# Optimization experiments

Measured on AMD Instinct MI355X. Metric: run time of the kernel, lower is better.

The kernel has to match this reference:

```python
import jax, jax.numpy as jnp
import numpy as np

B, T, E = 64, 512, 768
H = 512            # hid_dim
NF = 256           # n_filters
FS = (3, 4, 5)     # filter_sizes


def gru_step(x, h, Wih, Whh, bih, bhh):
    # torch.nn.GRUCell math; gate order: reset, update, new
    gi = x @ Wih.T + bih
    gh = h @ Whh.T + bhh
    ir, iz, in_ = jnp.split(gi, 3, axis=-1)
    hr, hz, hn = jnp.split(gh, 3, axis=-1)
    r = jax.nn.sigmoid(ir + hr)
    z = jax.nn.sigmoid(iz + hz)
    n = jnp.tanh(in_ + r * hn)
    return (1.0 - z) * n + z * h


def setup_inputs() -> dict:
    key = jax.random.key(0)
    ks = jax.random.split(key, 32)
    s = 0.02
    inp = {
        "embedded": jax.random.normal(ks[0], (B, T, E), jnp.float32),
        "mask": jnp.ones((B, T), jnp.int32),
        # select-policy GRUCell
        "Wih_c": jax.random.normal(ks[1], (3 * H, E)) * s,
        "Whh_c": jax.random.normal(ks[2], (3 * H, H)) * s,
        "bih_c": jnp.zeros((3 * H,)),
        "bhh_c": jnp.zeros((3 * H,)),
        "Ws": jax.random.normal(ks[3], (2, H)) * s,
        "bs": jnp.zeros((2,)),
        # 2-layer GRU
        "Wih0": jax.random.normal(ks[4], (3 * H, E)) * s,
        "Whh0": jax.random.normal(ks[5], (3 * H, H)) * s,
        "bih0": jnp.zeros((3 * H,)),
        "bhh0": jnp.zeros((3 * H,)),
        "Wih1": jax.random.normal(ks[6], (3 * H, H)) * s,
        "Whh1": jax.random.normal(ks[7], (3 * H, H)) * s,
        "bih1": jnp.zeros((3 * H,)),
        "bhh1": jnp.zeros((3 * H,)),
        # convs (OIHW)
        "Wc3": jax.random.normal(ks[8], (NF, 1, 3, H)) * s,
        "bc3": jnp.zeros((NF,)),
        "Wc4": jax.random.normal(ks[9], (NF, 1, 4, H)) * s,
        "bc4": jnp.zeros((NF,)),
        "Wc5": jax.random.normal(ks[10], (NF, 1, 5, H)) * s,
        "bc5": jnp.zeros((NF,)),
        # output linear
        "Wo": jax.random.normal(ks[11], (1, len(FS) * NF)) * s,
        "bo": jnp.zeros((1,)),
    }
    return inp


def reference(embedded, mask, Wih_c, Whh_c, bih_c, bhh_c, Ws, bs,
              Wih0, Whh0, bih0, bhh0, Wih1, Whh1, bih1, bhh1,
              Wc3, bc3, Wc4, bc4, Wc5, bc5, Wo, bo):
    b, t, _ = embedded.shape
    emb = jax.lax.stop_gradient(embedded)  # policy uses detached embeddings
    lens = mask.sum(axis=1).astype(jnp.int32)  # [B]

    # --- select_policy (eval mode: argmax selection), batched scan over time ---
    def sel_step(h, x_t):
        h = gru_step(x_t, h, Wih_c, Whh_c, bih_c, bhh_c)
        logits = h @ Ws.T + bs  # [B, 2]
        return h, jnp.argmax(logits, axis=-1).astype(jnp.int32)

    h0 = jnp.zeros((b, Whh_c.shape[1]), emb.dtype)
    _, ks = jax.lax.scan(sel_step, h0, jnp.swapaxes(emb, 0, 1))  # [T, B]
    sel = ks.T  # [B, T]
    t_idx = jnp.arange(t)[None, :]
    sel = jnp.where(t_idx == 0, 1, sel)                  # first token always kept
    sel = jnp.where(t_idx == lens[:, None] - 1, 1, sel)  # last valid token kept
    sel = jnp.where(t_idx >= lens[:, None], 0, sel)      # padding never kept
    nsel = sel.sum(axis=1)  # [B] lengths of compacted sequences

    # compact selected tokens to the front (stable argsort trick)
    order = jnp.argsort(1 - sel, axis=1, stable=True)  # [B, T]
    new_emb = jnp.take_along_axis(emb, order[:, :, None], axis=1)
    valid = t_idx < nsel[:, None]  # [B, T]
    new_emb = new_emb * valid[:, :, None].astype(emb.dtype)

    # --- 2-layer GRU over packed (= masked, left-aligned) sequences ---
    def run_layer(x, Wih, Whh, bih, bhh):
        def step(h, inputs):
            x_t, m_t = inputs
            hn = gru_step(x_t, h, Wih, Whh, bih, bhh)
            h = jnp.where(m_t[:, None], hn, h)
            return h, jnp.where(m_t[:, None], hn, jnp.zeros_like(hn))
        hh = jnp.zeros((x.shape[0], Whh.shape[1]), x.dtype)
        _, ys = jax.lax.scan(step, hh, (jnp.swapaxes(x, 0, 1), valid.T))
        return jnp.swapaxes(ys, 0, 1)  # [B, T, H]

    out = run_layer(new_emb, Wih0, Whh0, bih0, bhh0)
    out = run_layer(out, Wih1, Whh1, bih1, bhh1)

    # --- Kim-CNN head ---
    xc = out[:, None, :, :]  # [B, 1, T, H]
    pooled = []
    for Wc, bc in ((Wc3, bc3), (Wc4, bc4), (Wc5, bc5)):
        c = jax.lax.conv_general_dilated(
            xc, Wc, (1, 1), 'VALID',
            dimension_numbers=('NCHW', 'OIHW', 'NCHW'))  # [B, NF, T-fs+1, 1]
        c = jax.nn.relu(c + bc[None, :, None, None])[..., 0]
        pooled.append(jnp.max(c, axis=2))  # [B, NF]
    cat = jnp.concatenate(pooled, axis=1)  # dropout is identity in eval
    return (cat @ Wo.T + bo)[:, 0]  # [B]
```

## Files before the change

kernel.cpp:

```cpp
#include <hip/hip_runtime.h>
#include <hip/hip_bf16.h>
#include <cstddef>

constexpr int B_ = 64, T_ = 512, E_ = 768, H_ = 512, G_ = 1536, NF_ = 256;

typedef float f32x4 __attribute__((ext_vector_type(4)));
typedef __bf16 bf16x8 __attribute__((ext_vector_type(8)));

constexpr size_t SZ_GIC   = (size_t)B_ * T_ * G_ * 4;
constexpr size_t OFF_GI   = 0;
constexpr size_t OFF_OUT  = (size_t)B_ * T_ * G_ * 2;
constexpr size_t OFF_WBF0 = 170u * 1024 * 1024;
constexpr size_t OFF_WBF1 = OFF_WBF0 + (size_t)G_ * H_ * 2;
constexpr size_t OFF_WIH0 = OFF_WBF1 + (size_t)G_ * H_ * 2;
constexpr size_t OFF_WIH1 = OFF_WIH0 + (size_t)G_ * E_ * 2;
constexpr size_t OFF_WC3  = OFF_WIH1 + (size_t)G_ * H_ * 2;
constexpr size_t OFF_WC4  = OFF_WC3 + (size_t)NF_ * 3 * H_ * 2;
constexpr size_t OFF_WC5  = OFF_WC4 + (size_t)NF_ * 4 * H_ * 2;
constexpr size_t OFF_MISC = SZ_GIC;
constexpr size_t OFF_H0   = OFF_MISC;
constexpr size_t OFF_H1   = OFF_H0 + (size_t)B_ * H_ * 4;
constexpr size_t OFF_SEL  = OFF_H1 + (size_t)B_ * H_ * 4;
constexpr size_t OFF_ORD  = OFF_SEL + (size_t)B_ * T_ * 4;
constexpr size_t OFF_NSEL = OFF_ORD + (size_t)B_ * T_ * 4;
constexpr size_t OFF_MAXN = OFF_NSEL + 256;
constexpr size_t OFF_FLG  = OFF_MAXN + 256;
constexpr size_t OFF_JOBS = OFF_FLG + 512;
constexpr size_t OFF_POOL = OFF_FLG + 1024;
constexpr size_t OFF_RING0 = OFF_POOL + (size_t)B_ * 3 * NF_ * 4;
constexpr size_t OFF_RING1 = OFF_RING0 + 4ull * 64 * 512 * 2;
constexpr size_t WS_NEED  = OFF_RING1 + 4ull * 64 * 1536 * 2;

constexpr int WP_N0 = G_ * H_;
constexpr int WP_N1 = WP_N0 + G_ * H_;
constexpr int WP_N2 = WP_N1 + G_ * E_;
constexpr int WP_N3 = WP_N2 + G_ * H_;
constexpr int WP_N4 = WP_N3 + NF_ * 3 * H_;
constexpr int WP_N5 = WP_N4 + NF_ * 4 * H_;
constexpr int WP_N6 = WP_N5 + NF_ * 5 * H_;

#define CLOAD4(dst, ptr) \
    asm volatile("global_load_dwordx4 %0, %1, off sc0 sc1" : "=v"(dst) : "v"(ptr))
#define CLOAD2(dst, ptr) \
    asm volatile("global_load_dwordx2 %0, %1, off sc0 sc1" : "=v"(dst) : "v"(ptr))
#define CWAIT() do { \
    asm volatile("s_waitcnt vmcnt(0)" ::: "memory"); \
    __builtin_amdgcn_sched_barrier(0); } while (0)
#define CSTORE4(ptr, val) \
    asm volatile("global_store_dword %0, %1, off sc0 sc1" :: "v"(ptr), "v"(val) : "memory")
#define CSTORE8(ptr, val) \
    asm volatile("global_store_dwordx2 %0, %1, off sc0 sc1" :: "v"(ptr), "v"(val) : "memory")
#define CSTORE2(ptr, val) \
// ... 22 lines not shown
            __builtin_amdgcn_s_sleep(1);
        }
    }
    __syncthreads();
}

template<int N>
__device__ __forceinline__ void poll_ge(const int* flags, int thresh, int tid) {
    if (tid < 64) {
        const int idx = (tid < N) ? tid : 0;
        int v;
        for (;;) {
            asm volatile("global_load_dword %0, %1, off sc0 sc1\n\t"
                         "s_waitcnt vmcnt(0)"
                         : "=v"(v) : "v"(flags + idx) : "memory");
            if (__all(v >= thresh)) break;
            __builtin_amdgcn_s_sleep(1);
        }
    }
    __syncthreads();
}

__device__ __forceinline__ void poll_cnt(const int* p, int thr) {
    int v;
    for (;;) {
        asm volatile("global_load_dword %0, %1, off sc0 sc1\n\t"
                     "s_waitcnt vmcnt(0)"
                     : "=v"(v) : "v"(p) : "memory");
        if (__all(v >= thr)) break;
        __builtin_amdgcn_s_sleep(1);
    }
}

__device__ __forceinline__ void bar_wait128(const int* flags, int t, int tid) {
    if (tid < 64) {
        int v1, v2;
        for (;;) {
            asm volatile("global_load_dword %0, %2, off sc0 sc1\n\t"
                         "global_load_dword %1, %3, off sc0 sc1\n\t"
                         "s_waitcnt vmcnt(0)"
                         : "=&v"(v1), "=&v"(v2)
                         : "v"(flags + tid), "v"(flags + tid + 64) : "memory");
            if (__all((v1 >= t) && (v2 >= t))) break;
            __builtin_amdgcn_s_sleep(1);
        }
    }
    __syncthreads();
}

__device__ __forceinline__ void bar_arrive(int* flags, int t, int tid, int idx) {
    asm volatile("s_waitcnt vmcnt(0)" ::: "memory");
    __syncthreads();
    if (tid == 0) { int pv = t + 1; CSTORE4(flags + idx, pv); }
}

template<int AMODE, int OMODE>
__global__ __launch_bounds__(256) void gemm_mfma(
    const float* __restrict__ A, const unsigned short* __restrict__ Wb,
    const float* __restrict__ bias,
    unsigned short* __restrict__ Cb, unsigned int* __restrict__ pool,
    int N, int K, int ldA, int rowsPerB, int tilesPerB, int nb,
    const int* __restrict__ order, const int* __restrict__ nsel, int poolOff)
{
    __shared__ __align__(16) unsigned short As[64][40];
    __shared__ __align__(16) unsigned short Bs[64][40];
    __shared__ const float* rowp[64];

    const int tid = threadIdx.x;
    const int l = tid & 63;
    const int q = tid >> 6;
    const int per = 16 * nb;
    const int id = blockIdx.x;
    const int sup = id / per, rr2 = id % per;
    const int mblk = sup * 16 + (rr2 & 15);
    const int n0 = (rr2 >> 4) * 64;

    int tileb = 0, tilet0 = 0;
    if (AMODE != 0) { tileb = mblk / tilesPerB; tilet0 = (mblk % tilesPerB) * 64; }

    if (tid < 64) {
        const float* p = nullptr;
        if (AMODE == 0) {
            p = A + ((size_t)mblk * 64 + tid) * (size_t)ldA;
        } else if (AMODE == 1) {
            int t = tilet0 + tid;
            if (t < nsel[tileb]) {
                int src = order[tileb * T_ + t];
                p = A + ((size_t)tileb * T_ + src) * (size_t)ldA;
            }
        } else {
            int t = tilet0 + tid;
            if (t < rowsPerB) p = A + ((size_t)tileb * T_ + t) * (size_t)ldA;
        }
        rowp[tid] = p;
    }
    __syncthreads();

    f32x4 acc0 = {0.f,0.f,0.f,0.f}, acc1 = {0.f,0.f,0.f,0.f};
    f32x4 acc2 = {0.f,0.f,0.f,0.f}, acc3 = {0.f,0.f,0.f,0.f};

    const int r = tid & 63, seg = tid >> 6;
    const float* ap = rowp[r];
    if (ap) ap += seg * 8;
    const unsigned short* wrow = Wb + (size_t)(n0 + r) * (size_t)K + seg * 8;

    for (int k0 = 0; k0 < K; k0 += 32) {
        float4 fa = make_float4(0,0,0,0), fb = make_float4(0,0,0,0);
        if (ap) { fa = *(const float4*)(ap + k0); fb = *(const float4*)(ap + k0 + 4); }
        const uint4 wv = *(const uint4*)(wrow + k0);
        __syncthreads();
        uint4 pk;
        pk.x = (unsigned)f2bu(fa.x) | ((unsigned)f2bu(fa.y) << 16);
        pk.y = (unsigned)f2bu(fa.z) | ((unsigned)f2bu(fa.w) << 16);
        pk.z = (unsigned)f2bu(fb.x) | ((unsigned)f2bu(fb.y) << 16);
        pk.w = (unsigned)f2bu(fb.z) | ((unsigned)f2bu(fb.w) << 16);
        *(uint4*)&As[r][seg * 8] = pk;
        *(uint4*)&Bs[r][seg * 8] = wv;
        __syncthreads();
        const bf16x8 av = *(const bf16x8*)&As[q * 16 + (l & 15)][(l >> 4) * 8];
        const bf16x8 b0 = *(const bf16x8*)&Bs[ 0 + (l & 15)][(l >> 4) * 8];
        const bf16x8 b1 = *(const bf16x8*)&Bs[16 + (l & 15)][(l >> 4) * 8];
        const bf16x8 b2 = *(const bf16x8*)&Bs[32 + (l & 15)][(l >> 4) * 8];
// ... 8 lines not shown
    if (OMODE == 0) {
        const int mbase = (AMODE == 0) ? mblk * 64 : tileb * T_ + tilet0;
        #pragma unroll
        for (int s = 0; s < 4; ++s) {
            const int col = n0 + s * 16 + (l & 15);
            const float bv = bias[col];
            #pragma unroll
            for (int reg = 0; reg < 4; ++reg) {
                const int m = mbase + q * 16 + (l >> 4) * 4 + reg;
                Cb[(size_t)m * (size_t)N + col] = f2bu(accs[s][reg] + bv);
            }
        }
    } else {
        #pragma unroll
        for (int s = 0; s < 4; ++s) {
            const int col = n0 + s * 16 + (l & 15);
            const float bv = bias[col];
            float mx = 0.f;
            #pragma unroll
            for (int reg = 0; reg < 4; ++reg) {
                const int t = tilet0 + q * 16 + (l >> 4) * 4 + reg;
                const float val = fmaxf(accs[s][reg] + bv, 0.f);
                if (t < rowsPerB) mx = fmaxf(mx, val);
            }
            mx = fmaxf(mx, __shfl_xor(mx, 16));
            mx = fmaxf(mx, __shfl_xor(mx, 32));
            if (l < 16)
                atomicMax(&pool[(size_t)tileb * (3*NF_) + poolOff + n0 + s*16 + l],
                          __float_as_uint(mx));
        }
    }
}

__global__ void wprep_all(
    const float* __restrict__ w0, const float* __restrict__ w1,
    const float* __restrict__ w2, const float* __restrict__ w3,
    const float* __restrict__ w4, const float* __restrict__ w5,
    const float* __restrict__ w6, unsigned short* __restrict__ o)
{
    const int i = blockIdx.x * 256 + threadIdx.x;
    if (i >= WP_N6) return;
    float v;
    if      (i < WP_N0) v = w0[i];
    else if (i < WP_N1) v = w1[i - WP_N0];
    else if (i < WP_N2) v = w2[i - WP_N1];
    else if (i < WP_N3) v = w3[i - WP_N2];
    else if (i < WP_N4) v = w4[i - WP_N3];
    else if (i < WP_N5) v = w5[i - WP_N4];
    else                v = w6[i - WP_N5];
    o[i] = f2bu(v);
}

__device__ __forceinline__ void gates_abs(
    const float* __restrict__ hs, int b, int base,
    const float* __restrict__ wR, const float* __restrict__ wZ,
    const float* __restrict__ wN,
    float& aR, float& aZ, float& aN)
{
    #pragma unroll 4
    for (int kq = 0; kq < 32; ++kq) {
        const int k = base + kq * 4;
        const float hv0 = hs[(k+0)*64 + b];
        const float hv1 = hs[(k+1)*64 + b];
        const float hv2 = hs[(k+2)*64 + b];
        const float hv3 = hs[(k+3)*64 + b];
        const float4 wr = *(const float4*)(wR + k);
        const float4 wz = *(const float4*)(wZ + k);
        const float4 wn = *(const float4*)(wN + k);
        aR = fmaf(hv0, wr.x, aR); aR = fmaf(hv1, wr.y, aR);
        aR = fmaf(hv2, wr.z, aR); aR = fmaf(hv3, wr.w, aR);
        aZ = fmaf(hv0, wz.x, aZ); aZ = fmaf(hv1, wz.y, aZ);
        aZ = fmaf(hv2, wz.z, aZ); aZ = fmaf(hv3, wz.w, aZ);
        aN = fmaf(hv0, wn.x, aN); aN = fmaf(hv1, wn.y, aN);
        aN = fmaf(hv2, wn.z, aN); aN = fmaf(hv3, wn.w, aN);
    }
}

__device__ __forceinline__ void dot_abs(
    const float* __restrict__ hs, int b, int base,
    const float* __restrict__ dWl, float& dot)
{
    #pragma unroll 4
    for (int kq = 0; kq < 16; ++kq) {
        const int k = base + kq * 4;
        const float hv0 = hs[(k+0)*64 + b];
        const float hv1 = hs[(k+1)*64 + b];
        const float hv2 = hs[(k+2)*64 + b];
        const float hv3 = hs[(k+3)*64 + b];
        const float4 dv = *(const float4*)(dWl + k);
        dot = fmaf(hv0, dv.x, dot); dot = fmaf(hv1, dv.y, dot);
        dot = fmaf(hv2, dv.z, dot); dot = fmaf(hv3, dv.w, dot);
    }
}

__global__ __launch_bounds__(512) void sel_fused(
    const float* __restrict__ emb, const float* __restrict__ Wih_c,
    const float* __restrict__ bih_c, float* __restrict__ giC,
    const float* __restrict__ Whh, const float* __restrict__ bhh,
    const float* __restrict__ Ws, const float* __restrict__ bs,
    float* __restrict__ h0, float* __restrict__ h1,
    unsigned long long* __restrict__ selm, int* __restrict__ flags,
    int* __restrict__ jobs)
{
    __shared__ __align__(16) char smem[162816];
    const int tid = threadIdx.x;
    const int bx = blockIdx.x;

    if (bx >= 128) {
        const int p = bx - 128;
        float* As = (float*)smem;
        float* Bs = As + 16 * 68;
        const int half = tid >> 8;
        const int t2 = tid & 255;
        const int srl = t2 >> 2, skl = (t2 & 3) * 4;
        const int ty = tid >> 4;
        const int tx = tid & 15;

        for (int c = 0; c < 8; ++c) {
            for (int j = p; j < 1536; j += 128) {
                const int b = j / 24, n = j % 24;
                const int mblk = b * 8 + c;
                const int n0 = n * 64;
                const float* src = (half == 0)
                    ? emb + ((size_t)mblk * 64 + srl) * (size_t)E_ + skl
                    : Wih_c + ((size_t)(n0 + srl)) * (size_t)E_ + skl;
                float* dl = (half == 0) ? As : Bs;

                float acc[2][4] = {};
                for (int k0 = 0; k0 < E_; k0 += 16) {
                    const float4 v = *(const float4*)(src + k0);
                    __syncthreads();
                    dl[(skl+0)*68 + srl] = v.x; dl[(skl+1)*68 + srl] = v.y;
                    dl[(skl+2)*68 + srl] = v.z; dl[(skl+3)*68 + srl] = v.w;
                    __syncthreads();
                    #pragma unroll
                    for (int kk = 0; kk < 16; ++kk) {
                        const float a0 = As[kk*68 + ty*2 + 0];
                        const float a1 = As[kk*68 + ty*2 + 1];
                        const float4 w4 = *(const float4*)&Bs[kk*68 + tx*4];
                        acc[0][0]=fmaf(a0,w4.x,acc[0][0]); acc[0][1]=fmaf(a0,w4.y,acc[0][1]);
                        acc[0][2]=fmaf(a0,w4.z,acc[0][2]); acc[0][3]=fmaf(a0,w4.w,acc[0][3]);
                        acc[1][0]=fmaf(a1,w4.x,acc[1][0]); acc[1][1]=fmaf(a1,w4.y,acc[1][1]);
                        acc[1][2]=fmaf(a1,w4.z,acc[1][2]); acc[1][3]=fmaf(a1,w4.w,acc[1][3]);
                    }
                }
                const float4 bv = *(const float4*)(bih_c + n0 + tx*4);
                f32x4 o0, o1;
                o0[0] = acc[0][0]+bv.x; o0[1] = acc[0][1]+bv.y;
                o0[2] = acc[0][2]+bv.z; o0[3] = acc[0][3]+bv.w;
                o1[0] = acc[1][0]+bv.x; o1[1] = acc[1][1]+bv.y;
                o1[2] = acc[1][2]+bv.z; o1[3] = acc[1][3]+bv.w;
                const float* d0 = giC + (size_t)(mblk * 64 + ty*2) * (size_t)G_ + n0 + tx*4;
                CSTOREX4(d0, o0);
                CSTOREX4(d0 + G_, o1);
                asm volatile("s_waitcnt vmcnt(0)" ::: "memory");
                __syncthreads();
                if (tid == 0)
                    __hip_atomic_fetch_add(jobs + c, 1, __ATOMIC_RELAXED,
                                           __HIP_MEMORY_SCOPE_AGENT);
                __syncthreads();
            }
        }
        return;
    }

    float* Wl    = (float*)smem;
    float* dWl   = Wl + 6144;
    float* hs    = dWl + 512;
    float* partR = hs + 32768;
    float* partZ = partR + 256;
    float* partN = partZ + 256;
    float* pdot  = partN + 256;

    const int b = tid & 63;
    const int w = __builtin_amdgcn_readfirstlane(tid >> 6);
    const int u = w >> 1, s = w & 1;
    const int iu = bx * 4 + u;

    for (int idx = tid; idx < 12 * 512; idx += 512) {
        int rr = idx >> 9, k = idx & 511;
        int ul = rr / 3, gate = rr - ul * 3;
        Wl[idx] = Whh[((size_t)gate * 512 + bx * 4 + ul) * 512 + k];
    }
    dWl[tid] = Ws[512 + tid] - Ws[tid];
    __syncthreads();

    const float bR = bhh[iu], bZ = bhh[512 + iu], bN = bhh[1024 + iu];
    const float db = bs[1] - bs[0];
    const float* __restrict__ wR = Wl + (u*3 + 0) * 512;
    const float* __restrict__ wZ = Wl + (u*3 + 1) * 512;
    const float* __restrict__ wN = Wl + (u*3 + 2) * 512;

    float pgR = 0.f, pgZ = 0.f, pgN = 0.f;
    int ready_chunk = 0;
    if (s == 0) {
        poll_cnt(jobs + 0, 1536);
        ready_chunk = 1;
        const float* gp = giC + (size_t)b * T_ * G_;
        asm volatile("global_load_dword %0, %3, off sc0 sc1\n\t"
                     "global_load_dword %1, %4, off sc0 sc1\n\t"
                     "global_load_dword %2, %5, off sc0 sc1\n\t"
                     "s_waitcnt vmcnt(0)"
                     : "=&v"(pgR), "=&v"(pgZ), "=&v"(pgN)
                     : "v"(gp + iu), "v"(gp + 512 + iu), "v"(gp + 1024 + iu)
                     : "memory");
    }

    for (int t = 0; t <= T_; ++t) {
        const bool comp = (t < T_);
        const float* hcur = (t & 1) ? h1 : h0;
        float* hnxt = (t & 1) ? h0 : h1;

        if (t > 0) bar_wait128(flags, t, tid);

        const float* hc = hcur + (size_t)tid * 4;
        float* hd = hs + tid * 4;
        float4 a0,a1,a2,a3,a4,a5,a6,a7,a8,a9,aa,ab,ac,ad,ae,af;
        CLOAD4(a0, hc +  0*2048); CLOAD4(a1, hc +  1*2048);
        CLOAD4(a2, hc +  2*2048); CLOAD4(a3, hc +  3*2048);
        CLOAD4(a4, hc +  4*2048); CLOAD4(a5, hc +  5*2048);
        CLOAD4(a6, hc +  6*2048); CLOAD4(a7, hc +  7*2048);
        CLOAD4(a8, hc +  8*2048); CLOAD4(a9, hc +  9*2048);
        CLOAD4(aa, hc + 10*2048); CLOAD4(ab, hc + 11*2048);
        CLOAD4(ac, hc + 12*2048); CLOAD4(ad, hc + 13*2048);
        CLOAD4(ae, hc + 14*2048); CLOAD4(af, hc + 15*2048);
        CWAIT();
        *(float4*)(hd +  0*2048) = a0; *(float4*)(hd +  1*2048) = a1;
        *(float4*)(hd +  2*2048) = a2; *(float4*)(hd +  3*2048) = a3;
        *(float4*)(hd +  4*2048) = a4; *(float4*)(hd +  5*2048) = a5;
        *(float4*)(hd +  6*2048) = a6; *(float4*)(hd +  7*2048) = a7;
        *(float4*)(hd +  8*2048) = a8; *(float4*)(hd +  9*2048) = a9;
// ... 5 lines not shown
        float aR = (s == 0) ? bR : 0.f;
        float aZ = (s == 0) ? bZ : 0.f;
        float aN = (s == 0) ? bN : 0.f;
        float dot = 0.f, hp = 0.f;

        if (comp) {
            gates_abs(hs, b, s * 128,       wR, wZ, wN, aR, aZ, aN);
            gates_abs(hs, b, 256 + s * 128, wR, wZ, wN, aR, aZ, aN);
            if (s == 0) hp = hs[iu * 64 + b];
        }
        dot_abs(hs, b, (w < 4) ? w * 64 : 256 + (w - 4) * 64, dWl, dot);

        if (comp && s == 1) {
            partR[u*64 + b] = aR; partZ[u*64 + b] = aZ; partN[u*64 + b] = aN;
        }
        pdot[w*64 + b] = dot;
        __syncthreads();

        if (comp && s == 0) {
            aR += partR[u*64 + b]; aZ += partZ[u*64 + b]; aN += partN[u*64 + b];
            const float r = sigm(pgR + aR);
            const float z = sigm(pgZ + aZ);
            const float n = tanhf(pgN + r * aN);
            const float hn = (1.f - z) * n + z * hp;
            const float* hdst = hnxt + (size_t)iu * 64 + b;
            CSTORE4(hdst, hn);
        }

        if (t < T_) {
            bar_arrive(flags, t, tid, bx);
            if (s == 0 && t + 1 < T_) {
                const int nc = (t + 1) >> 6;
                if (nc >= ready_chunk) { poll_cnt(jobs + nc, 1536); ready_chunk = nc + 1; }
                const float* gp = giC + ((size_t)b * T_ + t + 1) * G_;
                asm volatile("global_load_dword %0, %3, off sc0 sc1\n\t"
                             "global_load_dword %1, %4, off sc0 sc1\n\t"
                             "global_load_dword %2, %5, off sc0 sc1\n\t"
                             "s_waitcnt vmcnt(0)"
                             : "=&v"(pgR), "=&v"(pgZ), "=&v"(pgN)
                             : "v"(gp + iu), "v"(gp + 512 + iu), "v"(gp + 1024 + iu)
                             : "memory");
            }
        }
        if (w == 0 && t >= 1) {
            float p2 = pdot[0*64 + b];
            p2 += pdot[1*64 + b]; p2 += pdot[2*64 + b]; p2 += pdot[3*64 + b];
            p2 += pdot[4*64 + b]; p2 += pdot[5*64 + b]; p2 += pdot[6*64 + b];
            p2 += pdot[7*64 + b];
            unsigned long long m = __ballot((p2 + db) > 0.f);
            if (tid == 0 && bx == 0) selm[t - 1] = m;
        }
    }
}

template<int ROLE>
__device__ __forceinline__ void layer_body(
    int wg, int tid,
    const unsigned short* __restrict__ gi0,
    const unsigned short* __restrict__ ring1,
    unsigned short* __restrict__ ring0,
    const unsigned short* __restrict__ wbf, const float* __restrict__ bhh,
    const int* __restrict__ nselp, const int* __restrict__ maxnp,
    unsigned short* __restrict__ hA, unsigned short* __restrict__ hB,
    float* __restrict__ outp,
    int* __restrict__ flagsSelf, const int* __restrict__ flagsB,
    unsigned char* ldsW, unsigned char* ldsH, float* gbuf)
{
    const int l = tid & 63;
    const int q = tid >> 6;
    const int i0 = wg * 16;
    const int b = tid & 63;

    for (int idx = tid; idx < 48 * 64; idx += 256) {
        const int r = idx >> 6, seg = idx & 63;
        const int tier = r >> 4, ul = r & 15;
        const float4 v = *(const float4*)((const char*)wbf
            + ((size_t)(tier * 512 + i0 + ul) * 512) * 2 + seg * 16);
        *(float4*)(ldsW + r * 1040 + seg * 16) = v;
    }
    const float4 bRv = *(const float4*)(bhh + i0 + 4 * q);
    const float4 bZv = *(const float4*)(bhh + 512 + i0 + 4 * q);
    const float4 bNv = *(const float4*)(bhh + 1024 + i0 + 4 * q);
    const int ns = nselp[b];
    const int TOTAL = *maxnp;

    const unsigned short* gbase = gi0 + (size_t)b * T_ * (size_t)G_ + i0 + 4 * q;
    uint2 gR, gZ, gN;
    if (ROLE == 0) {
        gR = *(const uint2*)(gbase);
        gZ = *(const uint2*)(gbase + 512);
        gN = *(const uint2*)(gbase + 1024);
    }
    __syncthreads();

    for (int t = 0; t < TOTAL; ++t) {
        const unsigned short* hcur = (t & 1) ? hB : hA;
        unsigned short* hnxt = (t & 1) ? hA : hB;

        if (t > 0) bar_wait<32>(flagsSelf, t, tid);
        if (ROLE == 0) {
            if (t >= 4) poll_ge<24>(flagsB, t - 3, tid);
        } else {
            poll_ge<24>(flagsB, t + 1, tid);
            const unsigned short* gp = ring1 + ((size_t)(t & 3) * 64 + b) * G_ + i0 + 4 * q;
            CLOAD2(gR, gp); CLOAD2(gZ, gp + 512); CLOAD2(gN, gp + 1024);
        }

        {
            const char* src = (const char*)hcur + tid * 256;
            float4 s0, s1, s2, s3, s4, s5, s6, s7, s8, s9, sa, sb_, sc, sd, se, sf;
            CLOAD4(s0, src + 0 * 16);  CLOAD4(s1, src + 1 * 16);
            CLOAD4(s2, src + 2 * 16);  CLOAD4(s3, src + 3 * 16);
            CLOAD4(s4, src + 4 * 16);  CLOAD4(s5, src + 5 * 16);
            CLOAD4(s6, src + 6 * 16);  CLOAD4(s7, src + 7 * 16);
            CLOAD4(s8, src + 8 * 16);  CLOAD4(s9, src + 9 * 16);
            CLOAD4(sa, src + 10 * 16); CLOAD4(sb_, src + 11 * 16);
            CLOAD4(sc, src + 12 * 16); CLOAD4(sd, src + 13 * 16);
            CLOAD4(se, src + 14 * 16); CLOAD4(sf, src + 15 * 16);
            CWAIT();
            char* dst = (char*)ldsH + (tid >> 2) * 1040 + (tid & 3) * 256;
            *(float4*)(dst + 0 * 16) = s0;  *(float4*)(dst + 1 * 16) = s1;
            *(float4*)(dst + 2 * 16) = s2;  *(float4*)(dst + 3 * 16) = s3;
            *(float4*)(dst + 4 * 16) = s4;  *(float4*)(dst + 5 * 16) = s5;
            *(float4*)(dst + 6 * 16) = s6;  *(float4*)(dst + 7 * 16) = s7;
// ... 46 lines not shown
            float4 o;
            unsigned short ob[4];
            #pragma unroll
            for (int j = 0; j < 4; ++j) {
                const int u2 = 4 * q + j;
                const float hr = gbuf[u2 * 66 + b]        + bRv[j];
                const float hz = gbuf[(16 + u2) * 66 + b] + bZv[j];
                const float hn = gbuf[(32 + u2) * 66 + b] + bNv[j];
                const float rr = sigm(irv[j] + hr);
                const float zz = sigm(izv[j] + hz);
                const float nn = tanhf(inv[j] + rr * hn);
                const float hpf = b2f(hpb[j]);
                float hv = (1.f - zz) * nn + zz * hpf;
                if (t >= ns) hv = hpf;
                ((float*)&o)[j] = hv;
                ob[j] = f2bu(hv);
            }
            uint2 hpk;
            hpk.x = (unsigned)ob[0] | ((unsigned)ob[1] << 16);
            hpk.y = (unsigned)ob[2] | ((unsigned)ob[3] << 16);
            if (ROLE == 0) {
                const unsigned short* rdst = ring0 + ((size_t)(t & 3) * 64 + b) * 512 + i0 + 4 * q;
                CSTORE8(rdst, hpk);
            } else {
                if (t < ns)
                    *(float4*)(outp + ((size_t)b * T_ + t) * 512 + i0 + 4 * q) = o;
            }
            const unsigned short* hdst = hnxt + (size_t)b * 512 + i0 + 4 * q;
            CSTORE8(hdst, hpk);
        }

        bar_arrive(flagsSelf, t, tid, wg);
        if (ROLE == 0 && t + 1 < TOTAL) {
            const unsigned short* gp = gbase + (size_t)(t + 1) * G_;
            gR = *(const uint2*)gp;
            gZ = *(const uint2*)(gp + 512);
            gN = *(const uint2*)(gp + 1024);
        }
    }
}

__global__ __launch_bounds__(256) void rec_fused(
    const unsigned short* __restrict__ gi0,
    const unsigned short* __restrict__ wbf0,
    const unsigned short* __restrict__ wbf1,
    const unsigned short* __restrict__ wih1b,
    const float* __restrict__ bhh0, const float* __restrict__ bhh1,
    const float* __restrict__ bih1,
    const int* __restrict__ nselp, const int* __restrict__ maxnp,
    unsigned short* __restrict__ h0A, unsigned short* __restrict__ h1A,
    unsigned short* __restrict__ h0C, unsigned short* __restrict__ h1C,
    unsigned short* __restrict__ ring0, unsigned short* __restrict__ ring1,
    float* __restrict__ outp,
    int* __restrict__ flagsA, int* __restrict__ flagsB, int* __restrict__ flagsC)
{
    __shared__ __align__(16) unsigned char ldsX[64 * 1040];
    __shared__ __align__(16) unsigned char ldsY[64 * 1040];
    __shared__ float gbuf[48 * 66];

    const int tid = threadIdx.x;
    const int bx = blockIdx.x;

    if (bx < 32) {
        layer_body<0>(bx, tid, gi0, nullptr, ring0, wbf0, bhh0, nselp, maxnp,
                      h0A, h1A, nullptr, flagsA, flagsB, ldsX, ldsY, gbuf);
    } else if (bx < 56) {
        const int wg = bx - 32;
        const int l = tid & 63;
        const int q = tid >> 6;
        const int n0 = wg * 64;

        for (int idx = tid; idx < 64 * 64; idx += 256) {
            const int r = idx >> 6, seg = idx & 63;
            const float4 v = *(const float4*)((const char*)wih1b
                + ((size_t)(n0 + r) * 512) * 2 + seg * 16);
            *(float4*)(ldsX + r * 1040 + seg * 16) = v;
        }
        float bv[4];
        #pragma unroll
        for (int s = 0; s < 4; ++s) bv[s] = bih1[n0 + s * 16 + (l & 15)];
        const int TOTAL = *maxnp;
        __syncthreads();

        for (int t = 0; t < TOTAL; ++t) {
            poll_ge<32>(flagsA, t + 1, tid);
            if (t >= 4) poll_ge<32>(flagsC, t - 3, tid);

            {
                const char* src = (const char*)ring0 + (size_t)(t & 3) * 65536 + tid * 256;
                float4 s0, s1, s2, s3, s4, s5, s6, s7, s8, s9, sa, sb_, sc, sd, se, sf;
                CLOAD4(s0, src + 0 * 16);  CLOAD4(s1, src + 1 * 16);
                CLOAD4(s2, src + 2 * 16);  CLOAD4(s3, src + 3 * 16);
                CLOAD4(s4, src + 4 * 16);  CLOAD4(s5, src + 5 * 16);
                CLOAD4(s6, src + 6 * 16);  CLOAD4(s7, src + 7 * 16);
                CLOAD4(s8, src + 8 * 16);  CLOAD4(s9, src + 9 * 16);
                CLOAD4(sa, src + 10 * 16); CLOAD4(sb_, src + 11 * 16);
                CLOAD4(sc, src + 12 * 16); CLOAD4(sd, src + 13 * 16);
// ... 14 lines not shown
            f32x4 acc0 = {0.f,0.f,0.f,0.f}, acc1 = {0.f,0.f,0.f,0.f};
            f32x4 acc2 = {0.f,0.f,0.f,0.f}, acc3 = {0.f,0.f,0.f,0.f};
            {
                const char* ab2 = (const char*)ldsY + (q * 16 + (l & 15)) * 1040 + (l >> 4) * 16;
                const char* bb = (const char*)ldsX + (l & 15) * 1040 + (l >> 4) * 16;
                #pragma unroll
                for (int ks = 0; ks < 16; ++ks) {
                    const bf16x8 av = *(const bf16x8*)(ab2 + ks * 64);
                    const bf16x8 b0 = *(const bf16x8*)(bb + ks * 64);
                    const bf16x8 b1 = *(const bf16x8*)(bb + 16 * 1040 + ks * 64);
                    const bf16x8 b2 = *(const bf16x8*)(bb + 32 * 1040 + ks * 64);
                    const bf16x8 b3 = *(const bf16x8*)(bb + 48 * 1040 + ks * 64);
                    acc0 = __builtin_amdgcn_mfma_f32_16x16x32_bf16(av, b0, acc0, 0, 0, 0);
                    acc1 = __builtin_amdgcn_mfma_f32_16x16x32_bf16(av, b1, acc1, 0, 0, 0);
                    acc2 = __builtin_amdgcn_mfma_f32_16x16x32_bf16(av, b2, acc2, 0, 0, 0);
                    acc3 = __builtin_amdgcn_mfma_f32_16x16x32_bf16(av, b3, acc3, 0, 0, 0);
                }
            }
            f32x4 accs[4] = {acc0, acc1, acc2, acc3};
            #pragma unroll
            for (int s = 0; s < 4; ++s) {
                const int col = n0 + s * 16 + (l & 15);
                #pragma unroll
                for (int reg = 0; reg < 4; ++reg) {
                    const int m = q * 16 + (l >> 4) * 4 + reg;
                    const unsigned val = f2bu(accs[s][reg] + bv[s]);
                    const unsigned short* dst = ring1 + ((size_t)(t & 3) * 64 + m) * G_ + col;
                    CSTORE2(dst, val);
                }
            }
            bar_arrive(flagsB, t, tid, wg);
        }
    } else {
        layer_body<1>(bx - 56, tid, nullptr, ring1, nullptr, wbf1, bhh1, nselp, maxnp,
                      h0C, h1C, outp, flagsC, flagsB, ldsX, ldsY, gbuf);
    }
}

__global__ void build_order_k(const int* __restrict__ mask,
                              const unsigned long long* __restrict__ selm,
                              int* __restrict__ order, int* __restrict__ nsel,
                              int* __restrict__ maxn)
{
    const int b = threadIdx.x;
    int lens = 0;
    for (int t = 0; t < T_; ++t) lens += (mask[b * T_ + t] != 0);
    int cnt = 0;
    for (int t = 0; t < T_; ++t) {
        int s = (int)((selm[t] >> b) & 1ull);
        if (t == 0) s = 1;
        if (t == lens - 1) s = 1;
        if (t >= lens) s = 0;
        if (s) order[b * T_ + (cnt++)] = t;
    }
    nsel[b] = cnt;
    int c2 = cnt;
    for (int t = 0; t < T_; ++t) {
        int s = (int)((selm[t] >> b) & 1ull);
        if (t == 0) s = 1;
        if (t == lens - 1) s = 1;
        if (t >= lens) s = 0;
        if (!s) order[b * T_ + (c2++)] = t;
    }
    __shared__ int red[64];
    red[b] = cnt;
    __syncthreads();
    if (b == 0) {
// ... 16 lines not shown

extern "C" void kernel_launch(void* const* d_in, const int* in_sizes, int n_in,
                              void* d_out, int out_size, void* d_ws, size_t ws_size,
                              hipStream_t stream)
{
    (void)in_sizes; (void)n_in; (void)out_size;
    const float* emb   = (const float*)d_in[0];
    const int*   mask  = (const int*)d_in[1];
    const float* Wih_c = (const float*)d_in[2];
    const float* Whh_c = (const float*)d_in[3];
    const float* bih_c = (const float*)d_in[4];
    const float* bhh_c = (const float*)d_in[5];
    const float* Ws    = (const float*)d_in[6];
    const float* bs    = (const float*)d_in[7];
    const float* Wih0  = (const float*)d_in[8];
    const float* Whh0  = (const float*)d_in[9];
    const float* bih0  = (const float*)d_in[10];
    const float* bhh0  = (const float*)d_in[11];
    const float* Wih1  = (const float*)d_in[12];
    const float* Whh1  = (const float*)d_in[13];
    const float* bih1  = (const float*)d_in[14];
    const float* bhh1  = (const float*)d_in[15];
    const float* Wc3   = (const float*)d_in[16];
    const float* bc3   = (const float*)d_in[17];
    const float* Wc4   = (const float*)d_in[18];
    const float* bc4   = (const float*)d_in[19];
    const float* Wc5   = (const float*)d_in[20];
    const float* bc5   = (const float*)d_in[21];
    const float* Wo    = (const float*)d_in[22];
    const float* bo    = (const float*)d_in[23];

    if (ws_size < WS_NEED) return;
    char* ws = (char*)d_ws;
    float*          giC    = (float*)(ws + OFF_GI);
    unsigned short* giB    = (unsigned short*)(ws + OFF_GI);
    float*          outbuf = (float*)(ws + OFF_OUT);
    unsigned short* wpack  = (unsigned short*)(ws + OFF_WBF0);
    unsigned short* wbf0   = (unsigned short*)(ws + OFF_WBF0);
    unsigned short* wbf1   = (unsigned short*)(ws + OFF_WBF1);
    unsigned short* wih0b  = (unsigned short*)(ws + OFF_WIH0);
    unsigned short* wih1b  = (unsigned short*)(ws + OFF_WIH1);
    unsigned short* wc3b   = (unsigned short*)(ws + OFF_WC3);
    unsigned short* wc4b   = (unsigned short*)(ws + OFF_WC4);
    unsigned short* wc5b   = (unsigned short*)(ws + OFF_WC5);
    float*          h0f    = (float*)(ws + OFF_H0);
    float*          h1f    = (float*)(ws + OFF_H1);
    unsigned short* h0A    = (unsigned short*)(ws + OFF_H0);
    unsigned short* h1A    = (unsigned short*)(ws + OFF_H0 + 65536);
    unsigned short* h0C    = (unsigned short*)(ws + OFF_H0 + 131072);
    unsigned short* h1C    = (unsigned short*)(ws + OFF_H0 + 196608);
    unsigned long long* selm = (unsigned long long*)(ws + OFF_SEL);
    int*            order  = (int*)(ws + OFF_ORD);
    int*            nsel   = (int*)(ws + OFF_NSEL);
    int*            maxn   = (int*)(ws + OFF_MAXN);
    int*            flagsA = (int*)(ws + OFF_FLG);
    int*            flagsB = (int*)(ws + OFF_FLG + 128);
    int*            flagsC = (int*)(ws + OFF_FLG + 256);
    int*            jobs   = (int*)(ws + OFF_JOBS);
    unsigned int*   pool   = (unsigned int*)(ws + OFF_POOL);
    unsigned short* ring0  = (unsigned short*)(ws + OFF_RING0);
    unsigned short* ring1  = (unsigned short*)(ws + OFF_RING1);

    hipMemsetAsync(flagsA, 0, 1024, stream);
    hipMemsetAsync(h0f, 0, (size_t)B_ * H_ * 4, stream);
    sel_fused<<<256, 512, 0, stream>>>(emb, Wih_c, bih_c, giC, Whh_c, bhh_c,
                                       Ws, bs, h0f, h1f, selm, flagsA, jobs);
    build_order_k<<<1, 64, 0, stream>>>(mask, selm, order, nsel, maxn);
    wprep_all<<<(WP_N6 + 255) / 256, 256, 0, stream>>>(Whh0, Whh1, Wih0, Wih1,
                                                       Wc3, Wc4, Wc5, wpack);
    gemm_mfma<1,0><<<dim3(512 * 24), 256, 0, stream>>>(emb, wih0b, bih0, giB, nullptr,
                                                       G_, E_, E_, T_, 8, 24, order, nsel, 0);
    hipMemsetAsync(flagsA, 0, 512, stream);
    hipMemsetAsync(h0A, 0, 65536, stream);
    hipMemsetAsync(h0C, 0, 65536, stream);
    hipMemsetAsync(outbuf, 0, (size_t)B_ * T_ * H_ * 4, stream);
    rec_fused<<<88, 256, 0, stream>>>(giB, wbf0, wbf1, wih1b, bhh0, bhh1, bih1,
                                      nsel, maxn, h0A, h1A, h0C, h1C,
                                      ring0, ring1, outbuf, flagsA, flagsB, flagsC);
    hipMemsetAsync(pool, 0, (size_t)B_ * 3 * NF_ * 4, stream);
    gemm_mfma<2,1><<<dim3(512 * 4), 256, 0, stream>>>(outbuf, wc3b, bc3, nullptr, pool,
                                                      NF_, 3*H_, H_, 510, 8, 4, nullptr, nullptr, 0);
    gemm_mfma<2,1><<<dim3(512 * 4), 256, 0, stream>>>(outbuf, wc4b, bc4, nullptr, pool,
                                                      NF_, 4*H_, H_, 509, 8, 4, nullptr, nullptr, 256);
    gemm_mfma<2,1><<<dim3(512 * 4), 256, 0, stream>>>(outbuf, wc5b, bc5, nullptr, pool,
                                                      NF_, 5*H_, H_, 508, 8, 4, nullptr, nullptr, 512);
    final_k<<<1, 64, 0, stream>>>(pool, Wo, bo, (float*)d_out);
}
```

Before: 9.703 ms.

## Overlap layer-0 input projection and weight prep with select-policy recurrence

The producer blocks of sel_fused now compute the full layer-0 input projection (emb×Wih0, in FP32 FMA, stored as bf16) for every timestep and do the bf16 weight packing while the select-policy recurrence runs. This removes the separate wprep and gather MFMA GEMM launches. The select-policy input projection now goes into a 128-row-per-batch ring buffer, with producers waiting on recurrence progress flags before overwriting entries, which shrinks the workspace. Layer 0 then gathers its gi rows through the order index. The trade-offs are that all T rows are projected instead of only the selected ones, scalar FMA replaces MFMA for that GEMM, and the ring adds a producer-consumer dependency.

```diff
diff --git a/kernel.cpp b/kernel.cpp
--- a/kernel.cpp
+++ b/kernel.cpp
@@ -7,17 +7,17 @@
 typedef float f32x4 __attribute__((ext_vector_type(4)));
 typedef __bf16 bf16x8 __attribute__((ext_vector_type(8)));
 
-constexpr size_t SZ_GIC   = (size_t)B_ * T_ * G_ * 4;
-constexpr size_t OFF_GI   = 0;
-constexpr size_t OFF_OUT  = (size_t)B_ * T_ * G_ * 2;
-constexpr size_t OFF_WBF0 = 170u * 1024 * 1024;
+constexpr size_t OFF_RING_GI = 0;
+constexpr size_t OFF_OUT     = 0;
+constexpr size_t OFF_GIFULL  = 64ull * 1024 * 1024;
+constexpr size_t OFF_WBF0    = 160ull * 1024 * 1024;
 constexpr size_t OFF_WBF1 = OFF_WBF0 + (size_t)G_ * H_ * 2;
 constexpr size_t OFF_WIH0 = OFF_WBF1 + (size_t)G_ * H_ * 2;
 constexpr size_t OFF_WIH1 = OFF_WIH0 + (size_t)G_ * E_ * 2;
 constexpr size_t OFF_WC3  = OFF_WIH1 + (size_t)G_ * H_ * 2;
 constexpr size_t OFF_WC4  = OFF_WC3 + (size_t)NF_ * 3 * H_ * 2;
 constexpr size_t OFF_WC5  = OFF_WC4 + (size_t)NF_ * 4 * H_ * 2;
-constexpr size_t OFF_MISC = SZ_GIC;
+constexpr size_t OFF_MISC = 192ull * 1024 * 1024;
 constexpr size_t OFF_H0   = OFF_MISC;
 constexpr size_t OFF_H1   = OFF_H0 + (size_t)B_ * H_ * 4;
 constexpr size_t OFF_SEL  = OFF_H1 + (size_t)B_ * H_ * 4;
@@ -106,7 +106,7 @@
     }
 }
 
-__device__ __forceinline__ void bar_wait128(const int* flags, int t, int tid) {
+__device__ __forceinline__ void poll128_ge(const int* flags, int thr, int tid) {
     if (tid < 64) {
         int v1, v2;
         for (;;) {
@@ -115,11 +115,15 @@
                          "s_waitcnt vmcnt(0)"
                          : "=&v"(v1), "=&v"(v2)
                          : "v"(flags + tid), "v"(flags + tid + 64) : "memory");
-            if (__all((v1 >= t) && (v2 >= t))) break;
+            if (__all((v1 >= thr) && (v2 >= thr))) break;
             __builtin_amdgcn_s_sleep(1);
         }
     }
     __syncthreads();
+}
+
+__device__ __forceinline__ void bar_wait128(const int* flags, int t, int tid) {
+    poll128_ge(flags, t, tid);
 }
 
 __device__ __forceinline__ void bar_arrive(int* flags, int t, int tid, int idx) {
@@ -156,12 +160,6 @@
         const float* p = nullptr;
         if (AMODE == 0) {
             p = A + ((size_t)mblk * 64 + tid) * (size_t)ldA;
-        } else if (AMODE == 1) {
-            int t = tilet0 + tid;
-            if (t < nsel[tileb]) {
-                int src = order[tileb * T_ + t];
-                p = A + ((size_t)tileb * T_ + src) * (size_t)ldA;
-            }
         } else {
             int t = tilet0 + tid;
             if (t < rowsPerB) p = A + ((size_t)tileb * T_ + t) * (size_t)ldA;
@@ -236,23 +234,61 @@
     }
 }
 
-__global__ void wprep_all(
-    const float* __restrict__ w0, const float* __restrict__ w1,
-    const float* __restrict__ w2, const float* __restrict__ w3,
-    const float* __restrict__ w4, const float* __restrict__ w5,
-    const float* __restrict__ w6, unsigned short* __restrict__ o)
+template<bool TORING>
+__device__ __forceinline__ void prod_job(
+    int mblk, int n0, int ringRowBase,
+    const float* __restrict__ emb, const float* __restrict__ W,
+    const float* __restrict__ bias,
+    float* __restrict__ ring, unsigned short* __restrict__ full,
+    float* As, float* Bs, int tid)
 {
-    const int i = blockIdx.x * 256 + threadIdx.x;
-    if (i >= WP_N6) return;
-    float v;
-    if      (i < WP_N0) v = w0[i];
-    else if (i < WP_N1) v = w1[i - WP_N0];
-    else if (i < WP_N2) v = w2[i - WP_N1];
-    else if (i < WP_N3) v = w3[i - WP_N2];
-    else if (i < WP_N4) v = w4[i - WP_N3];
-    else if (i < WP_N5) v = w5[i - WP_N4];
-    else                v = w6[i - WP_N5];
-    o[i] = f2bu(v);
+    const int half = tid >> 8;
+    const int t2 = tid & 255;
+    const int srl = t2 >> 2, skl = (t2 & 3) * 4;
+    const int ty = tid >> 4, tx = tid & 15;
+    const float* src = (half == 0)
+        ? emb + ((size_t)mblk * 64 + srl) * (size_t)E_ + skl
+        : W + ((size_t)(n0 + srl)) * (size_t)E_ + skl;
+    float* dl = (half == 0) ? As : Bs;
+
+    float acc[2][4] = {};
+    for (int k0 = 0; k0 < E_; k0 += 16) {
+        const float4 v = *(const float4*)(src + k0);
+        __syncthreads();
+        dl[(skl+0)*68 + srl] = v.x; dl[(skl+1)*68 + srl] = v.y;
+        dl[(skl+2)*68 + srl] = v.z; dl[(skl+3)*68 + srl] = v.w;
+        __syncthreads();
+        #pragma unroll
+        for (int kk = 0; kk < 16; ++kk) {
+            const float a0 = As[kk*68 + ty*2 + 0];
+            const float a1 = As[kk*68 + ty*2 + 1];
+            const float4 w4 = *(const float4*)&Bs[kk*68 + tx*4];
+            acc[0][0]=fmaf(a0,w4.x,acc[0][0]); acc[0][1]=fmaf(a0,w4.y,acc[0][1]);
+            acc[0][2]=fmaf(a0,w4.z,acc[0][2]); acc[0][3]=fmaf(a0,w4.w,acc[0][3]);
+            acc[1][0]=fmaf(a1,w4.x,acc[1][0]); acc[1][1]=fmaf(a1,w4.y,acc[1][1]);
+            acc[1][2]=fmaf(a1,w4.z,acc[1][2]); acc[1][3]=fmaf(a1,w4.w,acc[1][3]);
+        }
+    }
+    const float4 bv = *(const float4*)(bias + n0 + tx*4);
+    if (TORING) {
+        f32x4 o0, o1;
+        o0[0] = acc[0][0]+bv.x; o0[1] = acc[0][1]+bv.y;
+        o0[2] = acc[0][2]+bv.z; o0[3] = acc[0][3]+bv.w;
+        o1[0] = acc[1][0]+bv.x; o1[1] = acc[1][1]+bv.y;
+        o1[2] = acc[1][2]+bv.z; o1[3] = acc[1][3]+bv.w;
+        const float* d0 = ring + (size_t)(ringRowBase + ty*2) * (size_t)G_ + n0 + tx*4;
+        CSTOREX4(d0, o0);
+        CSTOREX4(d0 + G_, o1);
+    } else {
+        ushort4 s0, s1;
+        s0.x = f2bu(acc[0][0]+bv.x); s0.y = f2bu(acc[0][1]+bv.y);
+        s0.z = f2bu(acc[0][2]+bv.z); s0.w = f2bu(acc[0][3]+bv.w);
+        s1.x = f2bu(acc[1][0]+bv.x); s1.y = f2bu(acc[1][1]+bv.y);
+        s1.z = f2bu(acc[1][2]+bv.z); s1.w = f2bu(acc[1][3]+bv.w);
+        unsigned short* d0 = full + (size_t)(mblk * 64 + ty*2) * (size_t)G_ + n0 + tx*4;
+        *(ushort4*)d0 = s0;
+        *(ushort4*)(d0 + G_) = s1;
+    }
 }
 
 __device__ __forceinline__ void gates_abs(
@@ -299,12 +335,18 @@
 
 __global__ __launch_bounds__(512) void sel_fused(
     const float* __restrict__ emb, const float* __restrict__ Wih_c,
-    const float* __restrict__ bih_c, float* __restrict__ giC,
+    const float* __restrict__ bih_c, float* __restrict__ ring,
     const float* __restrict__ Whh, const float* __restrict__ bhh,
     const float* __restrict__ Ws, const float* __restrict__ bs,
     float* __restrict__ h0, float* __restrict__ h1,
     unsigned long long* __restrict__ selm, int* __restrict__ flags,
-    int* __restrict__ jobs)
+    int* __restrict__ jobs,
+    const float* __restrict__ Wih0, const float* __restrict__ bih0,
+    unsigned short* __restrict__ giFull,
+    const float* __restrict__ Whh0, const float* __restrict__ Whh1,
+    const float* __restrict__ Wih1,
+    const float* __restrict__ Wc3, const float* __restrict__ Wc4,
+    const float* __restrict__ Wc5, unsigned short* __restrict__ wpack)
 {
     __shared__ __align__(16) char smem[162816];
     const int tid = threadIdx.x;
@@ -314,49 +356,12 @@
         const int p = bx - 128;
         float* As = (float*)smem;
         float* Bs = As + 16 * 68;
-        const int half = tid >> 8;
-        const int t2 = tid & 255;
-        const int srl = t2 >> 2, skl = (t2 & 3) * 4;
-        const int ty = tid >> 4;
-        const int tx = tid & 15;
-
-        for (int c = 0; c < 8; ++c) {
+
+        for (int c = 0; c < 2; ++c) {
             for (int j = p; j < 1536; j += 128) {
                 const int b = j / 24, n = j % 24;
-                const int mblk = b * 8 + c;
-                const int n0 = n * 64;
-                const float* src = (half == 0)
-                    ? emb + ((size_t)mblk * 64 + srl) * (size_t)E_ + skl
-                    : Wih_c + ((size_t)(n0 + srl)) * (size_t)E_ + skl;
-                float* dl = (half == 0) ? As : Bs;
-
-                float acc[2][4] = {};
-                for (int k0 = 0; k0 < E_; k0 += 16) {
-                    const float4 v = *(const float4*)(src + k0);
-                    __syncthreads();
-                    dl[(skl+0)*68 + srl] = v.x; dl[(skl+1)*68 + srl] = v.y;
-                    dl[(skl+2)*68 + srl] = v.z; dl[(skl+3)*68 + srl] = v.w;
-                    __syncthreads();
-                    #pragma unroll
-                    for (int kk = 0; kk < 16; ++kk) {
-                        const float a0 = As[kk*68 + ty*2 + 0];
-                        const float a1 = As[kk*68 + ty*2 + 1];
-                        const float4 w4 = *(const float4*)&Bs[kk*68 + tx*4];
-                        acc[0][0]=fmaf(a0,w4.x,acc[0][0]); acc[0][1]=fmaf(a0,w4.y,acc[0][1]);
-                        acc[0][2]=fmaf(a0,w4.z,acc[0][2]); acc[0][3]=fmaf(a0,w4.w,acc[0][3]);
-                        acc[1][0]=fmaf(a1,w4.x,acc[1][0]); acc[1][1]=fmaf(a1,w4.y,acc[1][1]);
-                        acc[1][2]=fmaf(a1,w4.z,acc[1][2]); acc[1][3]=fmaf(a1,w4.w,acc[1][3]);
-                    }
-                }
-                const float4 bv = *(const float4*)(bih_c + n0 + tx*4);
-                f32x4 o0, o1;
-                o0[0] = acc[0][0]+bv.x; o0[1] = acc[0][1]+bv.y;
-                o0[2] = acc[0][2]+bv.z; o0[3] = acc[0][3]+bv.w;
-                o1[0] = acc[1][0]+bv.x; o1[1] = acc[1][1]+bv.y;
-                o1[2] = acc[1][2]+bv.z; o1[3] = acc[1][3]+bv.w;
-                const float* d0 = giC + (size_t)(mblk * 64 + ty*2) * (size_t)G_ + n0 + tx*4;
-                CSTOREX4(d0, o0);
-                CSTOREX4(d0 + G_, o1);
+                prod_job<true>(b * 8 + c, n * 64, b * 128 + (c & 1) * 64,
+                               emb, Wih_c, bih_c, ring, nullptr, As, Bs, tid);
                 asm volatile("s_waitcnt vmcnt(0)" ::: "memory");
                 __syncthreads();
                 if (tid == 0)
@@ -364,6 +369,48 @@
                                            __HIP_MEMORY_SCOPE_AGENT);
                 __syncthreads();
             }
+        }
+        int fg = 0;
+        for (int c = 2; c < 8; ++c) {
+            if (fg < 8) {
+                for (int j = p; j < 1536; j += 128) {
+                    const int b = j / 24, n = j % 24;
+                    prod_job<false>(b * 8 + fg, n * 64, 0,
+                                    emb, Wih0, bih0, nullptr, giFull, As, Bs, tid);
+                }
+                ++fg;
+            }
+            poll128_ge(flags, 64 * (c - 1), tid);
+            for (int j = p; j < 1536; j += 128) {
+                const int b = j / 24, n = j % 24;
+                prod_job<true>(b * 8 + c, n * 64, b * 128 + (c & 1) * 64,
+                               emb, Wih_c, bih_c, ring, nullptr, As, Bs, tid);
+                asm volatile("s_waitcnt vmcnt(0)" ::: "memory");
+                __syncthreads();
+                if (tid == 0)
+                    __hip_atomic_fetch_add(jobs + c, 1, __ATOMIC_RELAXED,
+                                           __HIP_MEMORY_SCOPE_AGENT);
+                __syncthreads();
+            }
+        }
+        while (fg < 8) {
+            for (int j = p; j < 1536; j += 128) {
+                const int b = j / 24, n = j % 24;
+                prod_job<false>(b * 8 + fg, n * 64, 0,
+                                emb, Wih0, bih0, nullptr, giFull, As, Bs, tid);
+            }
+            ++fg;
+        }
+        for (int i = p * 512 + tid; i < WP_N6; i += 128 * 512) {
+            float v;
+            if      (i < WP_N0) v = Whh0[i];
+            else if (i < WP_N1) v = Whh1[i - WP_N0];
+            else if (i < WP_N2) v = Wih0[i - WP_N1];
+            else if (i < WP_N3) v = Wih1[i - WP_N2];
+            else if (i < WP_N4) v = Wc3[i - WP_N3];
+            else if (i < WP_N5) v = Wc4[i - WP_N4];
+            else                v = Wc5[i - WP_N5];
+            wpack[i] = f2bu(v);
         }
         return;
     }
@@ -400,7 +447,7 @@
     if (s == 0) {
         poll_cnt(jobs + 0, 1536);
         ready_chunk = 1;
-        const float* gp = giC + (size_t)b * T_ * G_;
+        const float* gp = ring + (size_t)(b * 128) * G_;
         asm volatile("global_load_dword %0, %3, off sc0 sc1\n\t"
                      "global_load_dword %1, %4, off sc0 sc1\n\t"
                      "global_load_dword %2, %5, off sc0 sc1\n\t"
@@ -472,7 +519,7 @@
             if (s == 0 && t + 1 < T_) {
                 const int nc = (t + 1) >> 6;
                 if (nc >= ready_chunk) { poll_cnt(jobs + nc, 1536); ready_chunk = nc + 1; }
-                const float* gp = giC + ((size_t)b * T_ + t + 1) * G_;
+                const float* gp = ring + (size_t)(b * 128 + ((t + 1) & 127)) * G_;
                 asm volatile("global_load_dword %0, %3, off sc0 sc1\n\t"
                              "global_load_dword %1, %4, off sc0 sc1\n\t"
                              "global_load_dword %2, %5, off sc0 sc1\n\t"
@@ -497,6 +544,7 @@
 __device__ __forceinline__ void layer_body(
     int wg, int tid,
     const unsigned short* __restrict__ gi0,
+    const int* __restrict__ order,
     const unsigned short* __restrict__ ring1,
     unsigned short* __restrict__ ring0,
     const unsigned short* __restrict__ wbf, const float* __restrict__ bhh,
@@ -524,12 +572,13 @@
     const int ns = nselp[b];
     const int TOTAL = *maxnp;
 
-    const unsigned short* gbase = gi0 + (size_t)b * T_ * (size_t)G_ + i0 + 4 * q;
     uint2 gR, gZ, gN;
     if (ROLE == 0) {
-        gR = *(const uint2*)(gbase);
-        gZ = *(const uint2*)(gbase + 512);
-        gN = *(const uint2*)(gbase + 1024);
+        const int oi = order[b * T_];
+        const unsigned short* gp = gi0 + ((size_t)b * T_ + oi) * (size_t)G_ + i0 + 4 * q;
+        gR = *(const uint2*)gp;
+        gZ = *(const uint2*)(gp + 512);
+        gN = *(const uint2*)(gp + 1024);
     }
     __syncthreads();
 
@@ -642,7 +691,8 @@
 
         bar_arrive(flagsSelf, t, tid, wg);
         if (ROLE == 0 && t + 1 < TOTAL) {
-            const unsigned short* gp = gbase + (size_t)(t + 1) * G_;
+            const int oi = order[b * T_ + (t + 1)];
+            const unsigned short* gp = gi0 + ((size_t)b * T_ + oi) * (size_t)G_ + i0 + 4 * q;
             gR = *(const uint2*)gp;
             gZ = *(const uint2*)(gp + 512);
             gN = *(const uint2*)(gp + 1024);
@@ -651,7 +701,7 @@
 }
 
 __global__ __launch_bounds__(256) void rec_fused(
-    const unsigned short* __restrict__ gi0,
+    const unsigned short* __restrict__ giFull, const int* __restrict__ order,
     const unsigned short* __restrict__ wbf0,
     const unsigned short* __restrict__ wbf1,
     const unsigned short* __restrict__ wih1b,
@@ -672,7 +722,7 @@
     const int bx = blockIdx.x;
 
     if (bx < 32) {
-        layer_body<0>(bx, tid, gi0, nullptr, ring0, wbf0, bhh0, nselp, maxnp,
+        layer_body<0>(bx, tid, giFull, order, nullptr, ring0, wbf0, bhh0, nselp, maxnp,
                       h0A, h1A, nullptr, flagsA, flagsB, ldsX, ldsY, gbuf);
     } else if (bx < 56) {
         const int wg = bx - 32;
@@ -753,7 +803,7 @@
             bar_arrive(flagsB, t, tid, wg);
         }
     } else {
-        layer_body<1>(bx - 56, tid, nullptr, ring1, nullptr, wbf1, bhh1, nselp, maxnp,
+        layer_body<1>(bx - 56, tid, nullptr, nullptr, ring1, nullptr, wbf1, bhh1, nselp, maxnp,
                       h0C, h1C, outp, flagsC, flagsB, ldsX, ldsY, gbuf);
     }
 }
@@ -836,13 +886,12 @@
 
     if (ws_size < WS_NEED) return;
     char* ws = (char*)d_ws;
-    float*          giC    = (float*)(ws + OFF_GI);
-    unsigned short* giB    = (unsigned short*)(ws + OFF_GI);
+    float*          ring   = (float*)(ws + OFF_RING_GI);
     float*          outbuf = (float*)(ws + OFF_OUT);
+    unsigned short* giFull = (unsigned short*)(ws + OFF_GIFULL);
     unsigned short* wpack  = (unsigned short*)(ws + OFF_WBF0);
     unsigned short* wbf0   = (unsigned short*)(ws + OFF_WBF0);
     unsigned short* wbf1   = (unsigned short*)(ws + OFF_WBF1);
-    unsigned short* wih0b  = (unsigned short*)(ws + OFF_WIH0);
     unsigned short* wih1b  = (unsigned short*)(ws + OFF_WIH1);
     unsigned short* wc3b   = (unsigned short*)(ws + OFF_WC3);
     unsigned short* wc4b   = (unsigned short*)(ws + OFF_WC4);
@@ -867,18 +916,17 @@
 
     hipMemsetAsync(flagsA, 0, 1024, stream);
     hipMemsetAsync(h0f, 0, (size_t)B_ * H_ * 4, stream);
-    sel_fused<<<256, 512, 0, stream>>>(emb, Wih_c, bih_c, giC, Whh_c, bhh_c,
-                                       Ws, bs, h0f, h1f, selm, flagsA, jobs);
+    sel_fused<<<256, 512, 0, stream>>>(emb, Wih_c, bih_c, ring, Whh_c, bhh_c,
+                                       Ws, bs, h0f, h1f, selm, flagsA, jobs,
+                                       Wih0, bih0, giFull,
+                                       Whh0, Whh1, Wih1, Wc3, Wc4, Wc5, wpack);
     build_order_k<<<1, 64, 0, stream>>>(mask, selm, order, nsel, maxn);
-    wprep_all<<<(WP_N6 + 255) / 256, 256, 0, stream>>>(Whh0, Whh1, Wih0, Wih1,
-                                                       Wc3, Wc4, Wc5, wpack);
-    gemm_mfma<1,0><<<dim3(512 * 24), 256, 0, stream>>>(emb, wih0b, bih0, giB, nullptr,
-                                                       G_, E_, E_, T_, 8, 24, order, nsel, 0);
     hipMemsetAsync(flagsA, 0, 512, stream);
     hipMemsetAsync(h0A, 0, 65536, stream);
     hipMemsetAsync(h0C, 0, 65536, stream);
     hipMemsetAsync(outbuf, 0, (size_t)B_ * T_ * H_ * 4, stream);
-    rec_fused<<<88, 256, 0, stream>>>(giB, wbf0, wbf1, wih1b, bhh0, bhh1, bih1,
+    rec_fused<<<88, 256, 0, stream>>>(giFull, order, wbf0, wbf1, wih1b,
+                                      bhh0, bhh1, bih1,
                                       nsel, maxn, h0A, h1A, h0C, h1C,
                                       ring0, ring1, outbuf, flagsA, flagsB, flagsC);
     hipMemsetAsync(pool, 0, (size_t)B_ * 3 * NF_ * 4, stream);
```

Result: slower. 11.46 ms (+18.1%).
